# Kernel tuning notes

Hardware: AMD Instinct MI355X
Metric: run time of the kernel (lower is better)

## Reference

```python
import jax, jax.numpy as jnp
import numpy as np

N_NODES = 100000
N_EDGES = 1600000
NUM_FEATURES = 512
HIDDEN = 128
NUM_CLASSES = 40


def setup_inputs() -> dict:
    key = jax.random.key(0)
    ks = jax.random.split(key, 6)
    x = jax.random.normal(ks[0], (N_NODES, NUM_FEATURES), dtype=jnp.float32)
    edge_index = jax.random.randint(ks[1], (2, N_EDGES), 0, N_NODES, dtype=jnp.int32)
    W1 = jax.random.normal(ks[2], (NUM_FEATURES, HIDDEN), dtype=jnp.float32) * 0.05
    b1 = jnp.zeros((HIDDEN,), dtype=jnp.float32)
    W2 = jax.random.normal(ks[3], (HIDDEN, NUM_CLASSES), dtype=jnp.float32) * 0.05
    b2 = jnp.zeros((NUM_CLASSES,), dtype=jnp.float32)
    return {"x": x, "edge_index": edge_index, "W1": W1, "b1": b1, "W2": W2, "b2": b2}


def _gcn_conv(x, W, b, src, dst, n):
    # PyG GCNConv: h = W x; out = D^{-1/2} (A + I) D^{-1/2} h + b
    h = x @ W                                            # [N, out]
    deg = jax.ops.segment_sum(jnp.ones(src.shape[0], h.dtype), dst,
                              num_segments=n) + 1.0      # +1 for self loop
    inv_sqrt = jax.lax.rsqrt(deg)                        # [N]
    coef = inv_sqrt[src] * inv_sqrt[dst]                 # [E]
    msgs = h[src] * coef[:, None]                        # [E, out] gather
    agg = jax.ops.segment_sum(msgs, dst, num_segments=n) # scatter-add
    agg = agg + h * (inv_sqrt * inv_sqrt)[:, None]       # self-loop term
    return agg + b


def reference(x, edge_index, W1, b1, W2, b2):
    src, dst = edge_index[0], edge_index[1]
    n = x.shape[0]
    h = jax.nn.relu(_gcn_conv(x, W1, b1, src, dst, n))
    # F.dropout(training=self.training): eval mode -> identity
    out = _gcn_conv(h, W2, b2, src, dst, n)
    return jax.nn.log_softmax(out, axis=1)
```

## Files before the change

kernel.cpp:

```cpp
#include <hip/hip_runtime.h>
#include <hip/hip_bf16.h>
#include <math.h>

#define N_NODES 100000
#define N_EDGES 1600000
#define F_IN 512
#define HID 128
#define NCLS 40
#define DEG_CAP 64

typedef __attribute__((ext_vector_type(8))) short short8;
typedef __attribute__((ext_vector_type(4))) float floatx4;

__device__ __forceinline__ unsigned short f2bf(float x) {
    unsigned u = __builtin_bit_cast(unsigned, x);
    unsigned r = (u + 0x7FFFu + ((u >> 16) & 1u)) >> 16;
    return (unsigned short)r;
}
__device__ __forceinline__ float bflo(unsigned u) {
    return __builtin_bit_cast(float, u << 16);
}
__device__ __forceinline__ float bfhi(unsigned u) {
    return __builtin_bit_cast(float, u & 0xFFFF0000u);
}


__global__ void k_zero_int(int* p, int n) {
    int i = blockIdx.x * blockDim.x + threadIdx.x;
    if (i < n) p[i] = 0;
}


__global__ void k_fill_pad(const int* __restrict__ src, const int* __restrict__ dst,
                           int* __restrict__ cursor, int* __restrict__ csr, int e) {
    int i = blockIdx.x * blockDim.x + threadIdx.x;
    if (i >= e) return;
    int d = dst[i];
    int pos = atomicAdd(&cursor[d], 1);
    if (pos < DEG_CAP) csr[((size_t)d << 6) + pos] = src[i];
}

__global__ void k_inv(const int* __restrict__ deg, float* __restrict__ inv, int n) {
    int i = blockIdx.x * blockDim.x + threadIdx.x;
    if (i < n) inv[i] = rsqrtf((float)deg[i] + 1.0f);
}


__global__ __launch_bounds__(256) void k_wprep(
    const float* __restrict__ W1, unsigned short* __restrict__ W1t,
    const float* __restrict__ W2, unsigned short* __restrict__ W2th,
    unsigned short* __restrict__ W2tl) {
    int b = blockIdx.x;
    if (b < 256) {
        int idx = b * 256 + threadIdx.x;
        int n = idx >> 9, k = idx & 511;
        W1t[idx] = f2bf(W1[k * HID + n]);
    } else {
        int idx = (b - 256) * 256 + threadIdx.x;
        int n = idx >> 7, k = idx & 127;
        float v = (n < NCLS) ? W2[k * NCLS + n] : 0.f;
        unsigned short hi = f2bf(v);
        unsigned short lo = f2bf(v - bflo(hi));
        W2th[idx] = hi;
        W2tl[idx] = lo;
    }
}


#define GM 128

__global__ __launch_bounds__(256) void k_gemm1_mfma(
    const float* __restrict__ A,
    const unsigned short* __restrict__ Bt,
    const float* __restrict__ inv,
    unsigned short* __restrict__ C,
    int M)
{
    __shared__ unsigned short Asl[2][128 * 40];
    __shared__ unsigned short Bsl[2][128 * 40];

    const int tid  = threadIdx.x;
    const int wave = tid >> 6;
    const int lane = tid & 63;
    const int quad = lane >> 4;
    const int l15  = lane & 15;
    const int wm   = (wave >> 1) * 64;
    const int wn   = (wave & 1) * 64;
    const int block_m = blockIdx.x * GM;

    const int ra = tid >> 3, kqa = tid & 7;
    const int rb = tid >> 2, kqb = tid & 3;

    size_t aoff[4];
    #pragma unroll
    for (int i = 0; i < 4; ++i) {
        int gr = block_m + ra + 32 * i;
        gr = gr < M ? gr : M - 1;
        aoff[i] = (size_t)gr * F_IN + kqa * 4;
    }
    size_t boff[2];
    #pragma unroll
    for (int i = 0; i < 2; ++i)
        boff[i] = (size_t)(rb + 64 * i) * F_IN + kqb * 8;

    floatx4 areg[4];
    int4 breg[2];

    floatx4 acc[4][4];
    #pragma unroll
    for (int i = 0; i < 4; ++i)
        #pragma unroll
        for (int j = 0; j < 4; ++j) acc[i][j] = (floatx4){0.f, 0.f, 0.f, 0.f};

    #pragma unroll
    for (int i = 0; i < 4; ++i) areg[i] = *(const floatx4*)&A[aoff[i]];
    #pragma unroll
    for (int i = 0; i < 2; ++i) breg[i] = *(const int4*)&Bt[boff[i]];
    #pragma unroll
    for (int i = 0; i < 4; ++i) {
        floatx4 v = areg[i];
        unsigned lo = (unsigned)f2bf(v.x) | ((unsigned)f2bf(v.y) << 16);
        unsigned hi = (unsigned)f2bf(v.z) | ((unsigned)f2bf(v.w) << 16);
        *(uint2*)&Asl[0][(ra + 32 * i) * 40 + kqa * 4] = make_uint2(lo, hi);
    }
    #pragma unroll
    for (int i = 0; i < 2; ++i)
        *(int4*)&Bsl[0][(rb + 64 * i) * 40 + kqb * 8] = breg[i];
    __syncthreads();

    #pragma unroll 2
    for (int step = 0; step < 16; ++step) {
        const int buf = step & 1;

        if (step < 15) {
            const int k1 = (step + 1) * 32;
            #pragma unroll
            for (int i = 0; i < 4; ++i) areg[i] = *(const floatx4*)&A[aoff[i] + k1];
            #pragma unroll
            for (int i = 0; i < 2; ++i) breg[i] = *(const int4*)&Bt[boff[i] + k1];
        }

        short8 af[4], bfr[4];
        #pragma unroll
        for (int t = 0; t < 4; ++t)
            af[t] = *(const short8*)&Asl[buf][(wm + t * 16 + l15) * 40 + quad * 8];
        #pragma unroll
        for (int t = 0; t < 4; ++t)
            bfr[t] = *(const short8*)&Bsl[buf][(wn + t * 16 + l15) * 40 + quad * 8];

        #pragma unroll
        for (int tm = 0; tm < 4; ++tm)
            #pragma unroll
            for (int tn = 0; tn < 4; ++tn)
                acc[tm][tn] = __builtin_amdgcn_mfma_f32_16x16x32_bf16(
                    af[tm], bfr[tn], acc[tm][tn], 0, 0, 0);

        if (step < 15) {
            #pragma unroll
            for (int i = 0; i < 4; ++i) {
                floatx4 v = areg[i];
                unsigned lo = (unsigned)f2bf(v.x) | ((unsigned)f2bf(v.y) << 16);
                unsigned hi = (unsigned)f2bf(v.z) | ((unsigned)f2bf(v.w) << 16);
                *(uint2*)&Asl[buf ^ 1][(ra + 32 * i) * 40 + kqa * 4] = make_uint2(lo, hi);
            }
            #pragma unroll
            for (int i = 0; i < 2; ++i)
                *(int4*)&Bsl[buf ^ 1][(rb + 64 * i) * 40 + kqb * 8] = breg[i];
        }
        __syncthreads();
    }

    #pragma unroll
    for (int tm = 0; tm < 4; ++tm) {
        #pragma unroll
        for (int r = 0; r < 4; ++r) {
            int row = block_m + wm + tm * 16 + quad * 4 + r;
            if (row < M) {
                float iv = inv[row];
                #pragma unroll
                for (int tn = 0; tn < 4; ++tn)
                    C[(size_t)row * HID + wn + tn * 16 + l15] =
                        f2bf(acc[tm][tn][r] * iv);
            }
        }
    }
}


__global__ __launch_bounds__(256) void k_gather1(
    const unsigned* __restrict__ h1s,
    const int* __restrict__ deg,
    const float* __restrict__ inv, const int* __restrict__ csr,
    const float* __restrict__ b1, float* __restrict__ hrelu)
{
    const int wave = threadIdx.x >> 6;
    const int lane = threadIdx.x & 63;
    const int node = blockIdx.x * 4 + wave;
    const int start = node << 6;
    int cnt = deg[node];
    cnt = cnt < DEG_CAP ? cnt : DEG_CAP;

    unsigned u = h1s[(size_t)node * 64 + lane];
    float acc0 = bflo(u), acc1 = bfhi(u);

    int t = 0;
    for (; t + 4 <= cnt; t += 4) {
        int s0 = csr[start + t + 0];
        int s1 = csr[start + t + 1];
        int s2 = csr[start + t + 2];
        int s3 = csr[start + t + 3];
        unsigned u0 = h1s[(size_t)s0 * 64 + lane];
        unsigned u1 = h1s[(size_t)s1 * 64 + lane];
        unsigned u2 = h1s[(size_t)s2 * 64 + lane];
        unsigned u3 = h1s[(size_t)s3 * 64 + lane];
        acc0 += (bflo(u0) + bflo(u1)) + (bflo(u2) + bflo(u3));
        acc1 += (bfhi(u0) + bfhi(u1)) + (bfhi(u2) + bfhi(u3));
    }
    for (; t < cnt; ++t) {
        int s = csr[start + t];
        unsigned uu = h1s[(size_t)s * 64 + lane];
        acc0 += bflo(uu);
        acc1 += bfhi(uu);
    }

    float invd = inv[node];
    float2 b = *(const float2*)&b1[lane * 2];
    float v0 = fmaxf(acc0 * invd + b.x, 0.f);
    float v1 = fmaxf(acc1 * invd + b.y, 0.f);
    *(float2*)&hrelu[(size_t)node * HID + lane * 2] = make_float2(v0, v1);
}


#define G2M 128

__global__ __launch_bounds__(256) void k_gemm2_mfma(
    const float* __restrict__ H,
    const unsigned short* __restrict__ Bh,
    const unsigned short* __restrict__ Bl,
    const float* __restrict__ inv,
    unsigned short* __restrict__ C,
    int M)
{
    __shared__ unsigned short Ahs[128 * 40];
    __shared__ unsigned short Als[128 * 40];
    __shared__ unsigned short Bhs[48 * 136];
    __shared__ unsigned short Bls[48 * 136];

    const int tid  = threadIdx.x;
    const int wave = tid >> 6;
    const int lane = tid & 63;
    const int quad = lane >> 4;
    const int l15  = lane & 15;
    const int wm   = wave * 32;
    const int block_m = blockIdx.x * G2M;

    for (int i = tid; i < 768; i += 256) {
        int n = i >> 4;
        int k = (i & 15) * 8;
        *(int4*)&Bhs[n * 136 + k] = *(const int4*)&Bh[n * 128 + k];
        *(int4*)&Bls[n * 136 + k] = *(const int4*)&Bl[n * 128 + k];
    }

    const int ra = tid >> 3, kqa = tid & 7;
    size_t aoff[4];
    #pragma unroll
    for (int i = 0; i < 4; ++i) {
        int gr = block_m + ra + 32 * i;
        gr = gr < M ? gr : M - 1;
        aoff[i] = (size_t)gr * HID + kqa * 4;
    }

    floatx4 hreg[4];
    #pragma unroll
    for (int i = 0; i < 4; ++i) hreg[i] = *(const floatx4*)&H[aoff[i]];

    floatx4 acc[2][3];
    #pragma unroll
    for (int i = 0; i < 2; ++i)
        #pragma unroll
        for (int j = 0; j < 3; ++j) acc[i][j] = (floatx4){0.f, 0.f, 0.f, 0.f};

    for (int step = 0; step < 4; ++step) {
        #pragma unroll
        for (int i = 0; i < 4; ++i) {
            floatx4 v = hreg[i];
            unsigned short hx = f2bf(v.x), hy = f2bf(v.y);
            unsigned short hz = f2bf(v.z), hw = f2bf(v.w);
            unsigned short lx = f2bf(v.x - bflo(hx));
            unsigned short ly = f2bf(v.y - bflo(hy));
            unsigned short lz = f2bf(v.z - bflo(hz));
            unsigned short lw = f2bf(v.w - bflo(hw));
            *(uint2*)&Ahs[(ra + 32 * i) * 40 + kqa * 4] =
                make_uint2((unsigned)hx | ((unsigned)hy << 16),
                           (unsigned)hz | ((unsigned)hw << 16));
            *(uint2*)&Als[(ra + 32 * i) * 40 + kqa * 4] =
                make_uint2((unsigned)lx | ((unsigned)ly << 16),
                           (unsigned)lz | ((unsigned)lw << 16));
        }
        __syncthreads();

        if (step < 3) {
            const int k1 = (step + 1) * 32;
            #pragma unroll
            for (int i = 0; i < 4; ++i) hreg[i] = *(const floatx4*)&H[aoff[i] + k1];
        }

        const int k0 = step * 32;
        short8 ah[2], al[2], bh[3], bl[3];
        #pragma unroll
        for (int t = 0; t < 2; ++t) {
            ah[t] = *(const short8*)&Ahs[(wm + t * 16 + l15) * 40 + quad * 8];
            al[t] = *(const short8*)&Als[(wm + t * 16 + l15) * 40 + quad * 8];
        }
        #pragma unroll
        for (int t = 0; t < 3; ++t) {
            bh[t] = *(const short8*)&Bhs[(t * 16 + l15) * 136 + k0 + quad * 8];
            bl[t] = *(const short8*)&Bls[(t * 16 + l15) * 136 + k0 + quad * 8];
        }

        #pragma unroll
        for (int tm = 0; tm < 2; ++tm)
            #pragma unroll
            for (int tn = 0; tn < 3; ++tn) {
                acc[tm][tn] = __builtin_amdgcn_mfma_f32_16x16x32_bf16(
                    ah[tm], bh[tn], acc[tm][tn], 0, 0, 0);
                acc[tm][tn] = __builtin_amdgcn_mfma_f32_16x16x32_bf16(
                    al[tm], bh[tn], acc[tm][tn], 0, 0, 0);
                acc[tm][tn] = __builtin_amdgcn_mfma_f32_16x16x32_bf16(
                    ah[tm], bl[tn], acc[tm][tn], 0, 0, 0);
            }
        __syncthreads();
    }

    #pragma unroll
    for (int tm = 0; tm < 2; ++tm) {
        #pragma unroll
        for (int r = 0; r < 4; ++r) {
            int row = block_m + wm + tm * 16 + quad * 4 + r;
            if (row < M) {
                float iv = inv[row];
                #pragma unroll
                for (int tn = 0; tn < 3; ++tn) {
                    int col = tn * 16 + l15;
                    if (col < NCLS)
                        C[(size_t)row * NCLS + col] = f2bf(acc[tm][tn][r] * iv);
                }
            }
        }
    }
}


__global__ __launch_bounds__(256) void k_gather2(
    const unsigned* __restrict__ h2s,
    const int* __restrict__ deg,
    const float* __restrict__ inv, const int* __restrict__ csr,
    const float* __restrict__ b2, float* __restrict__ out)
{
    const int wave = threadIdx.x >> 6;
    const int lane = threadIdx.x & 63;
    const int node = blockIdx.x * 4 + wave;
    const int g = lane / 20;
    const int j = lane - g * 20;
    const int start = node << 6;
    int cnt = deg[node];
    cnt = cnt < DEG_CAP ? cnt : DEG_CAP;

    float acc0 = 0.f, acc1 = 0.f;
    if (g == 0) {
        unsigned u = h2s[(size_t)node * 20 + j];
        acc0 = bflo(u);
        acc1 = bfhi(u);
    }
    if (g < 3) {
        int t = g;
        for (; t + 3 < cnt; t += 6) {
            int s0 = csr[start + t];
            int s1 = csr[start + t + 3];
            unsigned u0 = h2s[(size_t)s0 * 20 + j];
            unsigned u1 = h2s[(size_t)s1 * 20 + j];
            acc0 += bflo(u0) + bflo(u1);
            acc1 += bfhi(u0) + bfhi(u1);
        }
        if (t < cnt) {
            int s = csr[start + t];
            unsigned u = h2s[(size_t)s * 20 + j];
            acc0 += bflo(u);
            acc1 += bfhi(u);
        }
    }
    acc0 += __shfl(acc0, j + 20) + __shfl(acc0, j + 40);
    acc1 += __shfl(acc1, j + 20) + __shfl(acc1, j + 40);

    float invd = inv[node];
    float v0 = -INFINITY, v1 = -INFINITY;
    if (g == 0) {
        float2 b = *(const float2*)&b2[j * 2];
        v0 = acc0 * invd + b.x;
        v1 = acc1 * invd + b.y;
    }
    float m = fmaxf(v0, v1);
    #pragma unroll
    for (int mask = 16; mask; mask >>= 1) m = fmaxf(m, __shfl_xor(m, mask));
    float e = (g == 0) ? (__expf(v0 - m) + __expf(v1 - m)) : 0.f;
    #pragma unroll
    for (int mask = 16; mask; mask >>= 1) e += __shfl_xor(e, mask);
    if (g == 0) {
        float lg = __logf(e);
        *(float2*)&out[(size_t)node * NCLS + j * 2] =
            make_float2(v0 - m - lg, v1 - m - lg);
    }
}


extern "C" void kernel_launch(void* const* d_in, const int* in_sizes, int n_in,
                              void* d_out, int out_size, void* d_ws, size_t ws_size,
                              hipStream_t stream) {
    const float* x   = (const float*)d_in[0];
    const int*   ei  = (const int*)d_in[1];
    const float* W1  = (const float*)d_in[2];
    const float* b1  = (const float*)d_in[3];
    const float* W2  = (const float*)d_in[4];
    const float* b2  = (const float*)d_in[5];
    float* out = (float*)d_out;

    const int* src = ei;
    const int* dst = ei + N_EDGES;

    char* wsb = (char*)d_ws;
    float* inv      = (float*)wsb;
    float* slot1    = inv + 131072;
    float* hrelu    = slot1 + (size_t)N_NODES * HID;
    int*   cursor   = (int*)(hrelu + (size_t)N_NODES * HID);
    int*   csr_pad  = cursor + 131072;
    unsigned short* W1t  = (unsigned short*)(csr_pad + (size_t)N_NODES * DEG_CAP);
    unsigned short* W2th = W1t + (size_t)F_IN * HID;
    unsigned short* W2tl = W2th + 48 * 128;
    unsigned short* h1s_st = (unsigned short*)slot1;
    unsigned short* h2s_st = (unsigned short*)slot1;
    unsigned* h1s_ld = (unsigned*)slot1;
    unsigned* h2s_ld = (unsigned*)slot1;

    const int T = 256;
    const int NB = (N_NODES + 255) / 256;

    k_zero_int<<<NB, T, 0, stream>>>(cursor, N_NODES);
    k_fill_pad<<<N_EDGES / T, T, 0, stream>>>(src, dst, cursor, csr_pad, N_EDGES);
    k_inv<<<NB, T, 0, stream>>>(cursor, inv, N_NODES);

    k_wprep<<<280, T, 0, stream>>>(W1, W1t, W2, W2th, W2tl);

    k_gemm1_mfma<<<(N_NODES + GM - 1) / GM, T, 0, stream>>>(x, W1t, inv, h1s_st, N_NODES);
    k_gather1<<<N_NODES / 4, T, 0, stream>>>(h1s_ld, cursor, inv, csr_pad, b1, hrelu);

    k_gemm2_mfma<<<(N_NODES + G2M - 1) / G2M, T, 0, stream>>>(hrelu, W2th, W2tl, inv, h2s_st, N_NODES);
    k_gather2<<<N_NODES / 4, T, 0, stream>>>(h2s_ld, cursor, inv, csr_pad, b2, out);
}
```

Baseline: 583.9 us.

## Overlap CSR build with GEMM1 by fusing into one launch, move source scaling to gather

Merges the cursor zeroing into the weight-prep kernel. Puts the edge-scatter CSR build into extra blocks of the GEMM1 kernel, so the atomic-heavy scatter runs alongside the MFMA tiles. This is possible because GEMM1 no longer scales rows by inv_sqrt(deg); the gather now multiplies each neighbour by inv[src], at the cost of an extra per-edge load. The GEMM1 mainloop also drops register-prefetch double buffering for a simpler single-buffer load/sync loop, which may expose global load latency.

After: 523.7 us. 1.11x faster.

```diff
diff --git a/kernel.cpp b/kernel.cpp
--- a/kernel.cpp
+++ b/kernel.cpp
@@ -8,6 +8,8 @@
 #define HID 128
 #define NCLS 40
 #define DEG_CAP 64
+#define GM 128
+#define NGB 782
 
 typedef __attribute__((ext_vector_type(8))) short short8;
 typedef __attribute__((ext_vector_type(4))) float floatx4;
@@ -25,37 +27,16 @@
 }
 
 
-__global__ void k_zero_int(int* p, int n) {
-    int i = blockIdx.x * blockDim.x + threadIdx.x;
-    if (i < n) p[i] = 0;
-}
-
-
-__global__ void k_fill_pad(const int* __restrict__ src, const int* __restrict__ dst,
-                           int* __restrict__ cursor, int* __restrict__ csr, int e) {
-    int i = blockIdx.x * blockDim.x + threadIdx.x;
-    if (i >= e) return;
-    int d = dst[i];
-    int pos = atomicAdd(&cursor[d], 1);
-    if (pos < DEG_CAP) csr[((size_t)d << 6) + pos] = src[i];
-}
-
-__global__ void k_inv(const int* __restrict__ deg, float* __restrict__ inv, int n) {
-    int i = blockIdx.x * blockDim.x + threadIdx.x;
-    if (i < n) inv[i] = rsqrtf((float)deg[i] + 1.0f);
-}
-
-
-__global__ __launch_bounds__(256) void k_wprep(
+__global__ __launch_bounds__(256) void k_prep(
     const float* __restrict__ W1, unsigned short* __restrict__ W1t,
     const float* __restrict__ W2, unsigned short* __restrict__ W2th,
-    unsigned short* __restrict__ W2tl) {
+    unsigned short* __restrict__ W2tl, int* __restrict__ cursor) {
     int b = blockIdx.x;
     if (b < 256) {
         int idx = b * 256 + threadIdx.x;
         int n = idx >> 9, k = idx & 511;
         W1t[idx] = f2bf(W1[k * HID + n]);
-    } else {
+    } else if (b < 280) {
         int idx = (b - 256) * 256 + threadIdx.x;
         int n = idx >> 7, k = idx & 127;
         float v = (n < NCLS) ? W2[k * NCLS + n] : 0.f;
@@ -63,21 +44,31 @@
         unsigned short lo = f2bf(v - bflo(hi));
         W2th[idx] = hi;
         W2tl[idx] = lo;
-    }
-}
-
-
-#define GM 128
-
-__global__ __launch_bounds__(256) void k_gemm1_mfma(
+    } else {
+        int i = (b - 280) * 256 + threadIdx.x;
+        if (i < N_NODES) cursor[i] = 0;
+    }
+}
+
+
+__global__ __launch_bounds__(256) void k_fused_g1f(
     const float* __restrict__ A,
     const unsigned short* __restrict__ Bt,
-    const float* __restrict__ inv,
     unsigned short* __restrict__ C,
-    int M)
+    int M,
+    const int* __restrict__ src, const int* __restrict__ dst,
+    int* __restrict__ cursor, int* __restrict__ csr)
 {
-    __shared__ unsigned short Asl[2][128 * 40];
-    __shared__ unsigned short Bsl[2][128 * 40];
+    __shared__ unsigned short Asl[128 * 40];
+    __shared__ unsigned short Bsl[128 * 40];
+
+    if (blockIdx.x >= NGB) {
+        int i = (blockIdx.x - NGB) * 256 + threadIdx.x;
+        int d = dst[i];
+        int pos = atomicAdd(&cursor[d], 1);
+        if (pos < DEG_CAP) csr[((size_t)d << 6) + pos] = src[i];
+        return;
+    }
 
     const int tid  = threadIdx.x;
     const int wave = tid >> 6;
@@ -88,65 +79,42 @@
     const int wn   = (wave & 1) * 64;
     const int block_m = blockIdx.x * GM;
 
-    const int ra = tid >> 3, kqa = tid & 7;
-    const int rb = tid >> 2, kqb = tid & 3;
-
-    size_t aoff[4];
-    #pragma unroll
-    for (int i = 0; i < 4; ++i) {
-        int gr = block_m + ra + 32 * i;
-        gr = gr < M ? gr : M - 1;
-        aoff[i] = (size_t)gr * F_IN + kqa * 4;
-    }
-    size_t boff[2];
-    #pragma unroll
-    for (int i = 0; i < 2; ++i)
-        boff[i] = (size_t)(rb + 64 * i) * F_IN + kqb * 8;
-
-    floatx4 areg[4];
-    int4 breg[2];
-
     floatx4 acc[4][4];
     #pragma unroll
     for (int i = 0; i < 4; ++i)
         #pragma unroll
         for (int j = 0; j < 4; ++j) acc[i][j] = (floatx4){0.f, 0.f, 0.f, 0.f};
 
-    #pragma unroll
-    for (int i = 0; i < 4; ++i) areg[i] = *(const floatx4*)&A[aoff[i]];
-    #pragma unroll
-    for (int i = 0; i < 2; ++i) breg[i] = *(const int4*)&Bt[boff[i]];
-    #pragma unroll
-    for (int i = 0; i < 4; ++i) {
-        floatx4 v = areg[i];
-        unsigned lo = (unsigned)f2bf(v.x) | ((unsigned)f2bf(v.y) << 16);
-        unsigned hi = (unsigned)f2bf(v.z) | ((unsigned)f2bf(v.w) << 16);
-        *(uint2*)&Asl[0][(ra + 32 * i) * 40 + kqa * 4] = make_uint2(lo, hi);
-    }
-    #pragma unroll
-    for (int i = 0; i < 2; ++i)
-        *(int4*)&Bsl[0][(rb + 64 * i) * 40 + kqb * 8] = breg[i];
-    __syncthreads();
-
-    #pragma unroll 2
-    for (int step = 0; step < 16; ++step) {
-        const int buf = step & 1;
-
-        if (step < 15) {
-            const int k1 = (step + 1) * 32;
-            #pragma unroll
-            for (int i = 0; i < 4; ++i) areg[i] = *(const floatx4*)&A[aoff[i] + k1];
-            #pragma unroll
-            for (int i = 0; i < 2; ++i) breg[i] = *(const int4*)&Bt[boff[i] + k1];
-        }
+    for (int k0 = 0; k0 < F_IN; k0 += 32) {
+        #pragma unroll
+        for (int i = 0; i < 4; ++i) {
+            int f  = tid + 256 * i;
+            int r  = f >> 3;
+            int kq = f & 7;
+            int gr = block_m + r;
+            gr = gr < M ? gr : M - 1;
+            floatx4 v = *(const floatx4*)&A[(size_t)gr * F_IN + k0 + kq * 4];
+            unsigned lo = (unsigned)f2bf(v.x) | ((unsigned)f2bf(v.y) << 16);
+            unsigned hi = (unsigned)f2bf(v.z) | ((unsigned)f2bf(v.w) << 16);
+            *(uint2*)&Asl[r * 40 + kq * 4] = make_uint2(lo, hi);
+        }
+        #pragma unroll
+        for (int i = 0; i < 2; ++i) {
+            int f  = tid + 256 * i;
+            int r  = f >> 2;
+            int kq = f & 3;
+            int4 v = *(const int4*)&Bt[(size_t)r * F_IN + k0 + kq * 8];
+            *(int4*)&Bsl[r * 40 + kq * 8] = v;
+        }
+        __syncthreads();
 
         short8 af[4], bfr[4];
         #pragma unroll
         for (int t = 0; t < 4; ++t)
-            af[t] = *(const short8*)&Asl[buf][(wm + t * 16 + l15) * 40 + quad * 8];
+            af[t] = *(const short8*)&Asl[(wm + t * 16 + l15) * 40 + quad * 8];
         #pragma unroll
         for (int t = 0; t < 4; ++t)
-            bfr[t] = *(const short8*)&Bsl[buf][(wn + t * 16 + l15) * 40 + quad * 8];
+            bfr[t] = *(const short8*)&Bsl[(wn + t * 16 + l15) * 40 + quad * 8];
 
         #pragma unroll
         for (int tm = 0; tm < 4; ++tm)
@@ -154,19 +122,6 @@
             for (int tn = 0; tn < 4; ++tn)
                 acc[tm][tn] = __builtin_amdgcn_mfma_f32_16x16x32_bf16(
                     af[tm], bfr[tn], acc[tm][tn], 0, 0, 0);
-
-        if (step < 15) {
-            #pragma unroll
-            for (int i = 0; i < 4; ++i) {
-                floatx4 v = areg[i];
-                unsigned lo = (unsigned)f2bf(v.x) | ((unsigned)f2bf(v.y) << 16);
-                unsigned hi = (unsigned)f2bf(v.z) | ((unsigned)f2bf(v.w) << 16);
-                *(uint2*)&Asl[buf ^ 1][(ra + 32 * i) * 40 + kqa * 4] = make_uint2(lo, hi);
-            }
-            #pragma unroll
-            for (int i = 0; i < 2; ++i)
-                *(int4*)&Bsl[buf ^ 1][(rb + 64 * i) * 40 + kqb * 8] = breg[i];
-        }
         __syncthreads();
     }
 
@@ -176,14 +131,18 @@
         for (int r = 0; r < 4; ++r) {
             int row = block_m + wm + tm * 16 + quad * 4 + r;
             if (row < M) {
-                float iv = inv[row];
                 #pragma unroll
                 for (int tn = 0; tn < 4; ++tn)
                     C[(size_t)row * HID + wn + tn * 16 + l15] =
-                        f2bf(acc[tm][tn][r] * iv);
+                        f2bf(acc[tm][tn][r]);
             }
         }
     }
+}
+
+__global__ void k_inv(const int* __restrict__ deg, float* __restrict__ inv, int n) {
+    int i = blockIdx.x * blockDim.x + threadIdx.x;
+    if (i < n) inv[i] = rsqrtf((float)deg[i] + 1.0f);
 }
 
 
@@ -197,11 +156,12 @@
     const int lane = threadIdx.x & 63;
     const int node = blockIdx.x * 4 + wave;
     const int start = node << 6;
+    const float invd = inv[node];
     int cnt = deg[node];
     cnt = cnt < DEG_CAP ? cnt : DEG_CAP;
 
     unsigned u = h1s[(size_t)node * 64 + lane];
-    float acc0 = bflo(u), acc1 = bfhi(u);
+    float acc0 = bflo(u) * invd, acc1 = bfhi(u) * invd;
 
     int t = 0;
     for (; t + 4 <= cnt; t += 4) {
@@ -209,21 +169,22 @@
         int s1 = csr[start + t + 1];
         int s2 = csr[start + t + 2];
         int s3 = csr[start + t + 3];
+        float w0 = inv[s0], w1 = inv[s1], w2 = inv[s2], w3 = inv[s3];
         unsigned u0 = h1s[(size_t)s0 * 64 + lane];
         unsigned u1 = h1s[(size_t)s1 * 64 + lane];
         unsigned u2 = h1s[(size_t)s2 * 64 + lane];
         unsigned u3 = h1s[(size_t)s3 * 64 + lane];
-        acc0 += (bflo(u0) + bflo(u1)) + (bflo(u2) + bflo(u3));
-        acc1 += (bfhi(u0) + bfhi(u1)) + (bfhi(u2) + bfhi(u3));
+        acc0 += (bflo(u0) * w0 + bflo(u1) * w1) + (bflo(u2) * w2 + bflo(u3) * w3);
+        acc1 += (bfhi(u0) * w0 + bfhi(u1) * w1) + (bfhi(u2) * w2 + bfhi(u3) * w3);
     }
     for (; t < cnt; ++t) {
         int s = csr[start + t];
+        float w = inv[s];
         unsigned uu = h1s[(size_t)s * 64 + lane];
-        acc0 += bflo(uu);
-        acc1 += bfhi(uu);
-    }
-
-    float invd = inv[node];
+        acc0 += bflo(uu) * w;
+        acc1 += bfhi(uu) * w;
+    }
+
     float2 b = *(const float2*)&b1[lane * 2];
     float v0 = fmaxf(acc0 * invd + b.x, 0.f);
     float v1 = fmaxf(acc1 * invd + b.y, 0.f);
@@ -444,13 +405,13 @@
     const int T = 256;
     const int NB = (N_NODES + 255) / 256;
 
-    k_zero_int<<<NB, T, 0, stream>>>(cursor, N_NODES);
-    k_fill_pad<<<N_EDGES / T, T, 0, stream>>>(src, dst, cursor, csr_pad, N_EDGES);
+    k_prep<<<280 + NB, T, 0, stream>>>(W1, W1t, W2, W2th, W2tl, cursor);
+
+    k_fused_g1f<<<NGB + N_EDGES / T, T, 0, stream>>>(
+        x, W1t, h1s_st, N_NODES, src, dst, cursor, csr_pad);
+
     k_inv<<<NB, T, 0, stream>>>(cursor, inv, N_NODES);
 
-    k_wprep<<<280, T, 0, stream>>>(W1, W1t, W2, W2th, W2tl);
-
-    k_gemm1_mfma<<<(N_NODES + GM - 1) / GM, T, 0, stream>>>(x, W1t, inv, h1s_st, N_NODES);
     k_gather1<<<N_NODES / 4, T, 0, stream>>>(h1s_ld, cursor, inv, csr_pad, b1, hrelu);
 
     k_gemm2_mfma<<<(N_NODES + G2M - 1) / G2M, T, 0, stream>>>(hrelu, W2th, W2tl, inv, h2s_st, N_NODES);
```
